# Optimization experiments

Measured on AMD Instinct MI355X. Metric: run time of the kernel, lower is better.

The kernel has to match this reference:

```python
import jax, jax.numpy as jnp
import numpy as np

N = 100000
E = 3200000
IN_CH = 128
HID = 64


def gcn_conv(x, row, col, W, b, n_nodes):
    # PyG GCNConv: add self-loops, symmetric deg^-1/2 normalization,
    # out = scatter_add(norm * (x W)[row] -> col) + bias
    h = x @ W  # [N, out]
    sl = jnp.arange(n_nodes)
    r = jnp.concatenate([row, sl])
    c = jnp.concatenate([col, sl])
    deg = jax.ops.segment_sum(jnp.ones_like(c, dtype=h.dtype), c, num_segments=n_nodes)
    dinv = jnp.where(deg > 0, jax.lax.rsqrt(deg), 0.0)
    norm = dinv[r] * dinv[c]  # [E+N]
    msg = h[r] * norm[:, None]
    out = jax.ops.segment_sum(msg, c, num_segments=n_nodes)
    return out + b


def setup_inputs() -> dict:
    key = jax.random.key(0)
    ks = jax.random.split(key, 8)
    x = jax.random.normal(ks[0], (N, IN_CH), dtype=jnp.float32)
    edge_index = jax.random.randint(ks[1], (2, E), 0, N, dtype=jnp.int64)
    s = 1.0 / np.sqrt(HID)
    W1 = jax.random.normal(ks[2], (IN_CH, HID), dtype=jnp.float32) / np.sqrt(IN_CH)
    b1 = jnp.zeros((HID,), jnp.float32)
    W2 = jax.random.normal(ks[3], (HID, HID), dtype=jnp.float32) * s
    b2 = jnp.zeros((HID,), jnp.float32)
    Wd1 = jax.random.normal(ks[4], (HID, HID), dtype=jnp.float32) * s
    bd1 = jax.random.uniform(ks[5], (HID,), jnp.float32, -s, s)
    Wd2 = jax.random.normal(ks[6], (HID, IN_CH), dtype=jnp.float32) * s
    bd2 = jax.random.uniform(ks[7], (IN_CH,), jnp.float32, -s, s)
    return {"x": x, "edge_index": edge_index, "W1": W1, "b1": b1,
            "W2": W2, "b2": b2, "Wd1": Wd1, "bd1": bd1, "Wd2": Wd2, "bd2": bd2}


def reference(x, edge_index, W1, b1, W2, b2, Wd1, bd1, Wd2, bd2):
    row, col = edge_index[0], edge_index[1]
    h = jax.nn.relu(gcn_conv(x, row, col, W1, b1, N))
    node_representation = jax.nn.relu(gcn_conv(h, row, col, W2, b2, N))
    rec = jax.nn.relu(node_representation @ Wd1 + bd1)
    reconstructed_x = rec @ Wd2 + bd2
    edge_scores = jnp.sum(node_representation[row] * node_representation[col], axis=1)
    return (reconstructed_x, edge_scores, node_representation)
```

## Files before the change

### kernel.cpp

```cpp
#include <hip/hip_runtime.h>

__global__ void k_zero_i(int* __restrict__ p, int n) {
    int i = blockIdx.x * blockDim.x + threadIdx.x;
    if (i < n) p[i] = 0;
}
__global__ void k_zero_f(float* __restrict__ p, long n) {
    long i = blockIdx.x * (long)blockDim.x + threadIdx.x;
    if (i < n) p[i] = 0.0f;
}


#define CH 16384

__global__ void k_hist(const int* __restrict__ col, int* __restrict__ hist,
                       int e, int B, int nchunks) {
    extern __shared__ int lh[];
    for (int i = threadIdx.x; i < B; i += 256) lh[i] = 0;
    __syncthreads();
    const int base = blockIdx.x * CH;
    const int end = min(e, base + CH);
    for (int i = base + threadIdx.x; i < end; i += 256)
        atomicAdd(&lh[col[i] >> 9], 1);
    __syncthreads();
    for (int b = threadIdx.x; b < B; b += 256)
        hist[(long)b * nchunks + blockIdx.x] = lh[b];
}

__global__ void k_scan_tbl(int* __restrict__ hist, long T) {
    __shared__ int ws[1024];
    const int tid = threadIdx.x;
    const long per = (T + 1023) >> 10;
    const long s = tid * per;
    const long e2 = min(T, s + per);
    int sum = 0;
    for (long i = s; i < e2; ++i) sum += hist[i];
    ws[tid] = sum;
    __syncthreads();
    for (int off = 1; off < 1024; off <<= 1) {
        int add = (tid >= off) ? ws[tid - off] : 0;
        __syncthreads();
        ws[tid] += add;
        __syncthreads();
    }
    int run = ws[tid] - sum;
    for (long i = s; i < e2; ++i) { int t = hist[i]; hist[i] = run; run += t; }
}

__global__ void k_part2(const int* __restrict__ row, const int* __restrict__ col,
                        const int* __restrict__ hist, int2* __restrict__ eb,
                        int e, int B, int nchunks) {
    extern __shared__ int cur[];
    const int bId = blockIdx.x;
    for (int b = threadIdx.x; b < B; b += 256)
        cur[b] = hist[(long)b * nchunks + bId];
    __syncthreads();
    const int base = bId * CH;
    const int end = min(e, base + CH);
    for (int i = base + threadIdx.x; i < end; i += 256) {
        int c = col[i];
        int p = atomicAdd(&cur[c >> 9], 1);
        eb[p] = make_int2(row[i], ((c & 511) << 22) | i);
    }
}

__global__ void k_bucket_csr(const int2* __restrict__ eb, const int* __restrict__ hist,
                             int nchunks, int* __restrict__ srow, int* __restrict__ seid,
                             int* __restrict__ startp, float* __restrict__ dinv,
                             int n, int e, int B) {
    __shared__ int scnt[512];
    __shared__ int sex[512];
    const int b = blockIdx.x;
    const int tid = threadIdx.x;
    for (int i = tid; i < 512; i += 256) scnt[i] = 0;
    __syncthreads();
    const int s = hist[(long)b * nchunks];
    const int s1 = (b + 1 < B) ? hist[(long)(b + 1) * nchunks] : e;
    for (int i = s + tid; i < s1; i += 256)
        atomicAdd(&scnt[(eb[i].y >> 22) & 511], 1);
    __syncthreads();
    if (tid < 64) {
        int vals[8];
        int tot = 0;
        #pragma unroll
        for (int k = 0; k < 8; ++k) { vals[k] = scnt[tid * 8 + k]; tot += vals[k]; }
        int acc = tot;
        #pragma unroll
        for (int off = 1; off < 64; off <<= 1) {
            int t = __shfl_up(acc, off);
            if (tid >= off) acc += t;
        }
        int excl = acc - tot;
        #pragma unroll
        for (int k = 0; k < 8; ++k) {
            sex[tid * 8 + k] = excl;
            int node = b * 512 + tid * 8 + k;
            if (node < n) {
                startp[node] = s + excl;
                dinv[node] = rsqrtf((float)vals[k] + 1.0f);
            }
            excl += vals[k];
        }
    }
    if (b == 0 && tid == 0) startp[n] = e;
    __syncthreads();
    for (int i = tid; i < 512; i += 256) scnt[i] = sex[i];
    __syncthreads();
    for (int i = s + tid; i < s1; i += 256) {
        int2 r = eb[i];
        int cl = (r.y >> 22) & 511;
        int p = atomicAdd(&scnt[cl], 1);
        srow[s + p] = r.x;
        seid[s + p] = r.y & 0x3FFFFF;
    }
}

__global__ void k_deg_count(const int* __restrict__ col, int* __restrict__ cnt, int e) {
    int i = blockIdx.x * blockDim.x + threadIdx.x;
    if (i < e) atomicAdd(&cnt[col[i]], 1);
}
__global__ void k_dinv(const int* __restrict__ cnt, float* __restrict__ dinv, int n) {
    int i = blockIdx.x * blockDim.x + threadIdx.x;
    if (i < n) dinv[i] = rsqrtf((float)cnt[i] + 1.0f);
}

template<int K, int OUT, bool BIAS, bool RELU, bool SCALE>
__launch_bounds__(256)
__global__ void k_gemm(const float* __restrict__ in, const float* __restrict__ W,
                       const float* __restrict__ b, const float* __restrict__ scale,
                       float* __restrict__ out, int n) {
    constexpr int NPB = 1024 / OUT;
    constexpr int GS  = 256 / OUT;
    __shared__ float sW[K * OUT];
    __shared__ float sX[NPB][K + 4];

    const int tid  = threadIdx.x;
    const int base = blockIdx.x * NPB;

    for (int i = tid; i < K * OUT; i += 256) sW[i] = W[i];
    for (int i = tid; i < NPB * K; i += 256) {
        int m = i / K, k = i - m * K;
        int node = base + m;
        sX[m][k] = (node < n) ? in[(long)node * K + k] : 0.0f;
    }
    __syncthreads();

    const int ch = tid % OUT;
    const int g  = tid / OUT;

    float acc[4] = {0.f, 0.f, 0.f, 0.f};
    #pragma unroll 4
    for (int k = 0; k < K; k += 4) {
        float w0 = sW[(k + 0) * OUT + ch];
        float w1 = sW[(k + 1) * OUT + ch];
        float w2 = sW[(k + 2) * OUT + ch];
        float w3 = sW[(k + 3) * OUT + ch];
        #pragma unroll
        for (int j = 0; j < 4; ++j) {
            float4 x4 = *reinterpret_cast<const float4*>(&sX[g + j * GS][k]);
            acc[j] += x4.x * w0 + x4.y * w1 + x4.z * w2 + x4.w * w3;
        }
    }

    #pragma unroll
    for (int j = 0; j < 4; ++j) {
        int node = base + g + j * GS;
        if (node < n) {
            float v = acc[j];
            if (BIAS) v += b[ch];
            if (RELU) v = fmaxf(v, 0.0f);
            if (SCALE) v *= scale[node];
            out[(long)node * OUT + ch] = v;
        }
    }
}

__launch_bounds__(256)
__global__ void k_gather_conv(const int* __restrict__ start, const int* __restrict__ srow,
                              const float* __restrict__ hs, const float* __restrict__ dinv,
                              const float* __restrict__ b, float* __restrict__ out, int n) {
    int node = blockIdx.x * 4 + (threadIdx.x >> 6);
    if (node >= n) return;
    int lane = threadIdx.x & 63;
    int sub = lane & 15;
    int eg  = lane >> 4;
    const int s = start[node], e2 = start[node + 1];
    float ax = 0.f, ay = 0.f, az = 0.f, aw = 0.f;
    int j = s + eg;
    for (; j + 28 < e2; j += 32) {
        int r0 = srow[j];      int r1 = srow[j + 4];
        int r2 = srow[j + 8];  int r3 = srow[j + 12];
        int r4 = srow[j + 16]; int r5 = srow[j + 20];
        int r6 = srow[j + 24]; int r7 = srow[j + 28];
        float4 a0 = *reinterpret_cast<const float4*>(&hs[(long)r0 * 64 + sub * 4]);
        float4 a1 = *reinterpret_cast<const float4*>(&hs[(long)r1 * 64 + sub * 4]);
        float4 a2 = *reinterpret_cast<const float4*>(&hs[(long)r2 * 64 + sub * 4]);
        float4 a3 = *reinterpret_cast<const float4*>(&hs[(long)r3 * 64 + sub * 4]);
        float4 a4 = *reinterpret_cast<const float4*>(&hs[(long)r4 * 64 + sub * 4]);
        float4 a5 = *reinterpret_cast<const float4*>(&hs[(long)r5 * 64 + sub * 4]);
        float4 a6 = *reinterpret_cast<const float4*>(&hs[(long)r6 * 64 + sub * 4]);
        float4 a7 = *reinterpret_cast<const float4*>(&hs[(long)r7 * 64 + sub * 4]);
        ax += a0.x; ay += a0.y; az += a0.z; aw += a0.w;
        ax += a1.x; ay += a1.y; az += a1.z; aw += a1.w;
        ax += a2.x; ay += a2.y; az += a2.z; aw += a2.w;
        ax += a3.x; ay += a3.y; az += a3.z; aw += a3.w;
        ax += a4.x; ay += a4.y; az += a4.z; aw += a4.w;
        ax += a5.x; ay += a5.y; az += a5.z; aw += a5.w;
        ax += a6.x; ay += a6.y; az += a6.z; aw += a6.w;
        ax += a7.x; ay += a7.y; az += a7.z; aw += a7.w;
    }
    for (; j < e2; j += 4) {
        int r = srow[j];
        float4 a = *reinterpret_cast<const float4*>(&hs[(long)r * 64 + sub * 4]);
        ax += a.x; ay += a.y; az += a.z; aw += a.w;
    }
    ax += __shfl_xor(ax, 16); ay += __shfl_xor(ay, 16);
    az += __shfl_xor(az, 16); aw += __shfl_xor(aw, 16);
    ax += __shfl_xor(ax, 32); ay += __shfl_xor(ay, 32);
    az += __shfl_xor(az, 32); aw += __shfl_xor(aw, 32);
    if (eg == 0) {
        float4 self = *reinterpret_cast<const float4*>(&hs[(long)node * 64 + sub * 4]);
        float4 b4   = *reinterpret_cast<const float4*>(&b[sub * 4]);
        float d = dinv[node];
        float4 o;
        o.x = fmaxf((ax + self.x) * d + b4.x, 0.0f);
        o.y = fmaxf((ay + self.y) * d + b4.y, 0.0f);
        o.z = fmaxf((az + self.z) * d + b4.z, 0.0f);
        o.w = fmaxf((aw + self.w) * d + b4.w, 0.0f);
        *reinterpret_cast<float4*>(&out[(long)node * 64 + sub * 4]) = o;
    }
}

__launch_bounds__(256)
__global__ void k_edge_scores_csr(const int* __restrict__ start, const int* __restrict__ srow,
                                  const int* __restrict__ eid, const float* __restrict__ nr,
                                  float* __restrict__ out, int n) {
    int node = blockIdx.x * 4 + (threadIdx.x >> 6);
    if (node >= n) return;
    int lane = threadIdx.x & 63;
    int sub = lane & 15;
    int eg  = lane >> 4;
    float4 c4 = *reinterpret_cast<const float4*>(&nr[(long)node * 64 + sub * 4]);
    int s = start[node], e2 = start[node + 1];
    int j = s + eg;
    for (; j + 28 < e2; j += 32) {
        int r0 = srow[j];      int r1 = srow[j + 4];
        int r2 = srow[j + 8];  int r3 = srow[j + 12];
        int r4 = srow[j + 16]; int r5 = srow[j + 20];
        int r6 = srow[j + 24]; int r7 = srow[j + 28];
        float4 a0 = *reinterpret_cast<const float4*>(&nr[(long)r0 * 64 + sub * 4]);
        float4 a1 = *reinterpret_cast<const float4*>(&nr[(long)r1 * 64 + sub * 4]);
        float4 a2 = *reinterpret_cast<const float4*>(&nr[(long)r2 * 64 + sub * 4]);
        float4 a3 = *reinterpret_cast<const float4*>(&nr[(long)r3 * 64 + sub * 4]);
        float4 a4 = *reinterpret_cast<const float4*>(&nr[(long)r4 * 64 + sub * 4]);
        float4 a5 = *reinterpret_cast<const float4*>(&nr[(long)r5 * 64 + sub * 4]);
        float4 a6 = *reinterpret_cast<const float4*>(&nr[(long)r6 * 64 + sub * 4]);
        float4 a7 = *reinterpret_cast<const float4*>(&nr[(long)r7 * 64 + sub * 4]);
        float v0 = a0.x * c4.x + a0.y * c4.y + a0.z * c4.z + a0.w * c4.w;
        float v1 = a1.x * c4.x + a1.y * c4.y + a1.z * c4.z + a1.w * c4.w;
        float v2 = a2.x * c4.x + a2.y * c4.y + a2.z * c4.z + a2.w * c4.w;
        float v3 = a3.x * c4.x + a3.y * c4.y + a3.z * c4.z + a3.w * c4.w;
        float v4 = a4.x * c4.x + a4.y * c4.y + a4.z * c4.z + a4.w * c4.w;
        float v5 = a5.x * c4.x + a5.y * c4.y + a5.z * c4.z + a5.w * c4.w;
        float v6 = a6.x * c4.x + a6.y * c4.y + a6.z * c4.z + a6.w * c4.w;
        float v7 = a7.x * c4.x + a7.y * c4.y + a7.z * c4.z + a7.w * c4.w;
        v0 += __shfl_xor(v0, 1); v1 += __shfl_xor(v1, 1);
        v2 += __shfl_xor(v2, 1); v3 += __shfl_xor(v3, 1);
        v4 += __shfl_xor(v4, 1); v5 += __shfl_xor(v5, 1);
        v6 += __shfl_xor(v6, 1); v7 += __shfl_xor(v7, 1);
        v0 += __shfl_xor(v0, 2); v1 += __shfl_xor(v1, 2);
        v2 += __shfl_xor(v2, 2); v3 += __shfl_xor(v3, 2);
        v4 += __shfl_xor(v4, 2); v5 += __shfl_xor(v5, 2);
        v6 += __shfl_xor(v6, 2); v7 += __shfl_xor(v7, 2);
        v0 += __shfl_xor(v0, 4); v1 += __shfl_xor(v1, 4);
        v2 += __shfl_xor(v2, 4); v3 += __shfl_xor(v3, 4);
        v4 += __shfl_xor(v4, 4); v5 += __shfl_xor(v5, 4);
        v6 += __shfl_xor(v6, 4); v7 += __shfl_xor(v7, 4);
        v0 += __shfl_xor(v0, 8); v1 += __shfl_xor(v1, 8);
        v2 += __shfl_xor(v2, 8); v3 += __shfl_xor(v3, 8);
        v4 += __shfl_xor(v4, 8); v5 += __shfl_xor(v5, 8);
        v6 += __shfl_xor(v6, 8); v7 += __shfl_xor(v7, 8);
        if (sub == 0) {
            out[eid[j]]      = v0; out[eid[j + 4]]  = v1;
            out[eid[j + 8]]  = v2; out[eid[j + 12]] = v3;
            out[eid[j + 16]] = v4; out[eid[j + 20]] = v5;
            out[eid[j + 24]] = v6; out[eid[j + 28]] = v7;
        }
    }
    for (; j + 12 < e2; j += 16) {
        int r0 = srow[j];
        int r1 = srow[j + 4];
        int r2 = srow[j + 8];
        int r3 = srow[j + 12];
        float4 a0 = *reinterpret_cast<const float4*>(&nr[(long)r0 * 64 + sub * 4]);
        float4 a1 = *reinterpret_cast<const float4*>(&nr[(long)r1 * 64 + sub * 4]);
        float4 a2 = *reinterpret_cast<const float4*>(&nr[(long)r2 * 64 + sub * 4]);
        float4 a3 = *reinterpret_cast<const float4*>(&nr[(long)r3 * 64 + sub * 4]);
        float v0 = a0.x * c4.x + a0.y * c4.y + a0.z * c4.z + a0.w * c4.w;
        float v1 = a1.x * c4.x + a1.y * c4.y + a1.z * c4.z + a1.w * c4.w;
        float v2 = a2.x * c4.x + a2.y * c4.y + a2.z * c4.z + a2.w * c4.w;
        float v3 = a3.x * c4.x + a3.y * c4.y + a3.z * c4.z + a3.w * c4.w;
        v0 += __shfl_xor(v0, 1); v1 += __shfl_xor(v1, 1);
        v2 += __shfl_xor(v2, 1); v3 += __shfl_xor(v3, 1);
        v0 += __shfl_xor(v0, 2); v1 += __shfl_xor(v1, 2);
        v2 += __shfl_xor(v2, 2); v3 += __shfl_xor(v3, 2);
        v0 += __shfl_xor(v0, 4); v1 += __shfl_xor(v1, 4);
        v2 += __shfl_xor(v2, 4); v3 += __shfl_xor(v3, 4);
        v0 += __shfl_xor(v0, 8); v1 += __shfl_xor(v1, 8);
        v2 += __shfl_xor(v2, 8); v3 += __shfl_xor(v3, 8);
        if (sub == 0) {
            out[eid[j]]      = v0;
            out[eid[j + 4]]  = v1;
            out[eid[j + 8]]  = v2;
            out[eid[j + 12]] = v3;
        }
    }
    for (; j < e2; j += 4) {
        int r = srow[j];
        float4 a = *reinterpret_cast<const float4*>(&nr[(long)r * 64 + sub * 4]);
        float v = a.x * c4.x + a.y * c4.y + a.z * c4.z + a.w * c4.w;
        v += __shfl_xor(v, 1);
        v += __shfl_xor(v, 2);
        v += __shfl_xor(v, 4);
        v += __shfl_xor(v, 8);
        if (sub == 0) out[eid[j]] = v;
    }
}

__global__ void k_scatter_simple(const int* __restrict__ row, const int* __restrict__ col,
                                 const float* __restrict__ hs, float* __restrict__ acc, int e) {
    int t = blockIdx.x * blockDim.x + threadIdx.x;
    int lane = t & 63;
    int eidx = t >> 6;
    if (eidx >= e) return;
    int r = row[eidx], c = col[eidx];
    atomicAdd(&acc[(long)c * 64 + lane], hs[(long)r * 64 + lane]);
}
__global__ void k_epilogue2(float* __restrict__ acc, const float* __restrict__ hs,
                            const float* __restrict__ dinv, const float* __restrict__ b, int n) {
    int i = blockIdx.x * blockDim.x + threadIdx.x;
    if (i >= n * 64) return;
    int node = i >> 6, ch = i & 63;
    acc[i] = fmaxf(dinv[node] * (acc[i] + hs[i]) + b[ch], 0.0f);
}
__global__ void k_edge_scores_orig(const int* __restrict__ row, const int* __restrict__ col,
                                   const float* __restrict__ nr, float* __restrict__ out, int e) {
    int t = blockIdx.x * blockDim.x + threadIdx.x;
    int sub = t & 15;
    int eidx = t >> 4;
    if (eidx >= e) return;
    int r = row[eidx], c = col[eidx];
    float4 a  = *reinterpret_cast<const float4*>(&nr[(long)r * 64 + sub * 4]);
    float4 bb = *reinterpret_cast<const float4*>(&nr[(long)c * 64 + sub * 4]);
    float s = a.x * bb.x + a.y * bb.y + a.z * bb.z + a.w * bb.w;
    s += __shfl_xor(s, 1);
    s += __shfl_xor(s, 2);
    s += __shfl_xor(s, 4);
    s += __shfl_xor(s, 8);
    if (sub == 0) out[eidx] = s;
}

extern "C" void kernel_launch(void* const* d_in, const int* in_sizes, int n_in,
                              void* d_out, int out_size, void* d_ws, size_t ws_size,
                              hipStream_t stream) {
    const float* x   = (const float*)d_in[0];
    const int*   ei  = (const int*)d_in[1];
    const float* W1  = (const float*)d_in[2];
    const float* b1  = (const float*)d_in[3];
    const float* W2  = (const float*)d_in[4];
    const float* b2  = (const float*)d_in[5];
    const float* Wd1 = (const float*)d_in[6];
    const float* bd1 = (const float*)d_in[7];
    const float* Wd2 = (const float*)d_in[8];
    const float* bd2 = (const float*)d_in[9];

    const int N = in_sizes[0] / 128;
    const int E = in_sizes[1] / 2;
    const int* row = ei;
    const int* col = ei + E;
    const int n64 = N * 64;
    const int B = (N + 511) >> 9;
    const int nchunks = (E + CH - 1) / CH;

    float* recon_out  = (float*)d_out;
    float* escore_out = recon_out + (long)N * 128;
    float* nr_out     = escore_out + E;

    float* dinv = (float*)d_ws;
    float* buf1 = dinv + N;
    float* buf2 = buf1 + (long)N * 64;
    int* startp = (int*)(buf2 + (long)N * 64);
    int* srow   = startp + N + 1;
    int* seid   = srow + E;
    int* hist   = seid + E;
    int2* ebuck = (int2*)buf1;

    size_t need_full = sizeof(float) * ((size_t)N + 2uL * n64)
                     + sizeof(int) * ((size_t)N + 1 + 2uL * E + (size_t)B * nchunks);
    bool csr_ok = (ws_size >= need_full) && (E < (1 << 22)) && ((long)E * 2 <= (long)n64)
                  && (B <= 2048);

    if (csr_ok) {
        k_hist<<<nchunks, 256, B * sizeof(int), stream>>>(col, hist, E, B, nchunks);
        k_scan_tbl<<<1, 1024, 0, stream>>>(hist, (long)B * nchunks);
        k_part2<<<nchunks, 256, B * sizeof(int), stream>>>(row, col, hist, ebuck, E, B, nchunks);
        k_bucket_csr<<<B, 256, 0, stream>>>(ebuck, hist, nchunks, srow, seid, startp, dinv, N, E, B);

        k_gemm<128, 64, false, false, true><<<(N + 15) / 16, 256, 0, stream>>>(x, W1, nullptr, dinv, buf1, N);
        k_gather_conv<<<(N + 3) / 4, 256, 0, stream>>>(startp, srow, buf1, dinv, b1, buf2, N);
        k_gemm<64, 64, false, false, true><<<(N + 15) / 16, 256, 0, stream>>>(buf2, W2, nullptr, dinv, buf1, N);
        k_gather_conv<<<(N + 3) / 4, 256, 0, stream>>>(startp, srow, buf1, dinv, b2, nr_out, N);
        k_gemm<64, 64, true, true, false><<<(N + 15) / 16, 256, 0, stream>>>(nr_out, Wd1, bd1, nullptr, buf2, N);
        k_gemm<64, 128, true, false, false><<<(N + 7) / 8, 256, 0, stream>>>(buf2, Wd2, bd2, nullptr, recon_out, N);
        k_edge_scores_csr<<<(N + 3) / 4, 256, 0, stream>>>(startp, srow, seid, nr_out, escore_out, N);
    } else {
        int* cnt = startp;
        k_zero_i<<<(N + 255) / 256, 256, 0, stream>>>(cnt, N);
        k_deg_count<<<(E + 255) / 256, 256, 0, stream>>>(col, cnt, E);
        k_dinv<<<(N + 255) / 256, 256, 0, stream>>>(cnt, dinv, N);
        k_zero_f<<<(n64 + 255) / 256, 256, 0, stream>>>(buf2, n64);
        k_zero_f<<<(n64 + 255) / 256, 256, 0, stream>>>(nr_out, n64);

        k_gemm<128, 64, false, false, true><<<(N + 15) / 16, 256, 0, stream>>>(x, W1, nullptr, dinv, buf1, N);
        k_scatter_simple<<<((long)E * 64 + 255) / 256, 256, 0, stream>>>(row, col, buf1, buf2, E);
        k_epilogue2<<<(n64 + 255) / 256, 256, 0, stream>>>(buf2, buf1, dinv, b1, N);
        k_gemm<64, 64, false, false, true><<<(N + 15) / 16, 256, 0, stream>>>(buf2, W2, nullptr, dinv, buf1, N);
        k_scatter_simple<<<((long)E * 64 + 255) / 256, 256, 0, stream>>>(row, col, buf1, nr_out, E);
        k_epilogue2<<<(n64 + 255) / 256, 256, 0, stream>>>(nr_out, buf1, dinv, b2, N);
        k_gemm<64, 64, true, true, false><<<(N + 15) / 16, 256, 0, stream>>>(nr_out, Wd1, bd1, nullptr, buf2, N);
        k_gemm<64, 128, true, false, false><<<(N + 7) / 8, 256, 0, stream>>>(buf2, Wd2, bd2, nullptr, recon_out, N);
        k_edge_scores_orig<<<((long)E * 16 + 255) / 256, 256, 0, stream>>>(row, col, nr_out, escore_out, E);
    }
}
```

Measured before the change: 915.3 us.

## Fuse W2 GEMM into first gather-conv and fuse both decoder GEMMs

The second-layer weight multiply (W2, scaled by dinv) moves into the epilogue of the first aggregation kernel. Each block stages W2 in shared memory and multiplies its 4 aggregated rows there, which removes one intermediate round trip to global memory and one launch. The two decoder GEMMs are merged into one kernel that keeps the ReLU hidden layer in shared memory. The cost is that every 4-node gather block now reloads 16KB of W2 and every 8-node decoder block reloads 48KB of weights, which adds shared-memory and L2 traffic and may lower occupancy.

```diff
diff --git a/kernel.cpp b/kernel.cpp
--- a/kernel.cpp
+++ b/kernel.cpp
@@ -171,6 +171,85 @@
             if (SCALE) v *= scale[node];
             out[(long)node * OUT + ch] = v;
         }
+    }
+}
+
+__launch_bounds__(256)
+__global__ void k_gather_conv_w2(const int* __restrict__ start, const int* __restrict__ srow,
+                                 const float* __restrict__ hs, const float* __restrict__ dinv,
+                                 const float* __restrict__ b, const float* __restrict__ W2,
+                                 float* __restrict__ hs2, int n) {
+    __shared__ float sW[64 * 64];
+    __shared__ float srb[4][64];
+    const int tid = threadIdx.x;
+    for (int i = tid; i < 64 * 64; i += 256) sW[i] = W2[i];
+
+    const int wid = tid >> 6;
+    const int node = blockIdx.x * 4 + wid;
+    const bool valid = node < n;
+    const int lane = tid & 63;
+    const int sub = lane & 15;
+    const int eg  = lane >> 4;
+
+    int s = 0, e2 = 0;
+    if (valid) { s = start[node]; e2 = start[node + 1]; }
+    float ax = 0.f, ay = 0.f, az = 0.f, aw = 0.f;
+    int j = s + eg;
+    for (; j + 28 < e2; j += 32) {
+        int r0 = srow[j];      int r1 = srow[j + 4];
+        int r2 = srow[j + 8];  int r3 = srow[j + 12];
+        int r4 = srow[j + 16]; int r5 = srow[j + 20];
+        int r6 = srow[j + 24]; int r7 = srow[j + 28];
+        float4 a0 = *reinterpret_cast<const float4*>(&hs[(long)r0 * 64 + sub * 4]);
+        float4 a1 = *reinterpret_cast<const float4*>(&hs[(long)r1 * 64 + sub * 4]);
+        float4 a2 = *reinterpret_cast<const float4*>(&hs[(long)r2 * 64 + sub * 4]);
+        float4 a3 = *reinterpret_cast<const float4*>(&hs[(long)r3 * 64 + sub * 4]);
+        float4 a4 = *reinterpret_cast<const float4*>(&hs[(long)r4 * 64 + sub * 4]);
+        float4 a5 = *reinterpret_cast<const float4*>(&hs[(long)r5 * 64 + sub * 4]);
+        float4 a6 = *reinterpret_cast<const float4*>(&hs[(long)r6 * 64 + sub * 4]);
+        float4 a7 = *reinterpret_cast<const float4*>(&hs[(long)r7 * 64 + sub * 4]);
+        ax += a0.x; ay += a0.y; az += a0.z; aw += a0.w;
+        ax += a1.x; ay += a1.y; az += a1.z; aw += a1.w;
+        ax += a2.x; ay += a2.y; az += a2.z; aw += a2.w;
+        ax += a3.x; ay += a3.y; az += a3.z; aw += a3.w;
+        ax += a4.x; ay += a4.y; az += a4.z; aw += a4.w;
+        ax += a5.x; ay += a5.y; az += a5.z; aw += a5.w;
+        ax += a6.x; ay += a6.y; az += a6.z; aw += a6.w;
+        ax += a7.x; ay += a7.y; az += a7.z; aw += a7.w;
+    }
+    for (; j < e2; j += 4) {
+        int r = srow[j];
+        float4 a = *reinterpret_cast<const float4*>(&hs[(long)r * 64 + sub * 4]);
+        ax += a.x; ay += a.y; az += a.z; aw += a.w;
+    }
+    ax += __shfl_xor(ax, 16); ay += __shfl_xor(ay, 16);
+    az += __shfl_xor(az, 16); aw += __shfl_xor(aw, 16);
+    ax += __shfl_xor(ax, 32); ay += __shfl_xor(ay, 32);
+    az += __shfl_xor(az, 32); aw += __shfl_xor(aw, 32);
+
+    float d = valid ? dinv[node] : 0.f;
+    if (valid && eg == 0) {
+        float4 self = *reinterpret_cast<const float4*>(&hs[(long)node * 64 + sub * 4]);
+        float4 b4   = *reinterpret_cast<const float4*>(&b[sub * 4]);
+        float4 o;
+        o.x = fmaxf((ax + self.x) * d + b4.x, 0.0f);
+        o.y = fmaxf((ay + self.y) * d + b4.y, 0.0f);
+        o.z = fmaxf((az + self.z) * d + b4.z, 0.0f);
+        o.w = fmaxf((aw + self.w) * d + b4.w, 0.0f);
+        *reinterpret_cast<float4*>(&srb[wid][sub * 4]) = o;
+    }
+    __syncthreads();
+    if (valid) {
+        float acc = 0.f;
+        #pragma unroll 4
+        for (int k = 0; k < 64; k += 4) {
+            float4 r4 = *reinterpret_cast<const float4*>(&srb[wid][k]);
+            acc += r4.x * sW[(k + 0) * 64 + lane];
+            acc += r4.y * sW[(k + 1) * 64 + lane];
+            acc += r4.z * sW[(k + 2) * 64 + lane];
+            acc += r4.w * sW[(k + 3) * 64 + lane];
+        }
+        hs2[(long)node * 64 + lane] = acc * d;
     }
 }
 
@@ -227,6 +306,72 @@
         o.z = fmaxf((az + self.z) * d + b4.z, 0.0f);
         o.w = fmaxf((aw + self.w) * d + b4.w, 0.0f);
         *reinterpret_cast<float4*>(&out[(long)node * 64 + sub * 4]) = o;
+    }
+}
+
+__launch_bounds__(256)
+__global__ void k_decoder(const float* __restrict__ nr, const float* __restrict__ Wd1,
+                          const float* __restrict__ bd1, const float* __restrict__ Wd2,
+                          const float* __restrict__ bd2, float* __restrict__ recon, int n) {
+    __shared__ float sW1[64 * 64];
+    __shared__ float sW2d[64 * 128];
+    __shared__ float sX[8][68];
+    __shared__ float sR[8][68];
+    const int tid = threadIdx.x;
+    const int base = blockIdx.x * 8;
+    for (int i = tid; i < 64 * 64; i += 256) sW1[i] = Wd1[i];
+    for (int i = tid; i < 64 * 128; i += 256) sW2d[i] = Wd2[i];
+    for (int i = tid; i < 8 * 64; i += 256) {
+        int m = i >> 6, k = i & 63;
+        int node = base + m;
+        sX[m][k] = (node < n) ? nr[(long)node * 64 + k] : 0.0f;
+    }
+    __syncthreads();
+    {
+        const int ch = tid & 63;
+        const int g  = tid >> 6;
+        float acc0 = 0.f, acc1 = 0.f;
+        #pragma unroll 4
+        for (int k = 0; k < 64; k += 4) {
+            float w0 = sW1[(k + 0) * 64 + ch];
+            float w1 = sW1[(k + 1) * 64 + ch];
+            float w2 = sW1[(k + 2) * 64 + ch];
+            float w3 = sW1[(k + 3) * 64 + ch];
+            float4 x0 = *reinterpret_cast<const float4*>(&sX[g][k]);
+            float4 x1 = *reinterpret_cast<const float4*>(&sX[g + 4][k]);
+            acc0 += x0.x * w0 + x0.y * w1 + x0.z * w2 + x0.w * w3;
+            acc1 += x1.x * w0 + x1.y * w1 + x1.z * w2 + x1.w * w3;
+        }
+        float bb = bd1[ch];
+        sR[g][ch]     = fmaxf(acc0 + bb, 0.f);
+        sR[g + 4][ch] = fmaxf(acc1 + bb, 0.f);
+    }
+    __syncthreads();
+    {
+        const int ch = tid & 127;
+        const int g2 = tid >> 7;
+        float a0 = 0.f, a1 = 0.f, a2 = 0.f, a3 = 0.f;
+        #pragma unroll 4
+        for (int k = 0; k < 64; k += 4) {
+            float w0 = sW2d[(k + 0) * 128 + ch];
+            float w1 = sW2d[(k + 1) * 128 + ch];
+            float w2 = sW2d[(k + 2) * 128 + ch];
+            float w3 = sW2d[(k + 3) * 128 + ch];
+            float4 r0 = *reinterpret_cast<const float4*>(&sR[g2][k]);
+            float4 r1 = *reinterpret_cast<const float4*>(&sR[g2 + 2][k]);
+            float4 r2 = *reinterpret_cast<const float4*>(&sR[g2 + 4][k]);
+            float4 r3 = *reinterpret_cast<const float4*>(&sR[g2 + 6][k]);
+            a0 += r0.x * w0 + r0.y * w1 + r0.z * w2 + r0.w * w3;
+            a1 += r1.x * w0 + r1.y * w1 + r1.z * w2 + r1.w * w3;
+            a2 += r2.x * w0 + r2.y * w1 + r2.z * w2 + r2.w * w3;
+            a3 += r3.x * w0 + r3.y * w1 + r3.z * w2 + r3.w * w3;
+        }
+        float bb = bd2[ch];
+        int n0 = base + g2;
+        if (n0 < n)     recon[(long)n0 * 128 + ch]       = a0 + bb;
+        if (n0 + 2 < n) recon[(long)(n0 + 2) * 128 + ch] = a1 + bb;
+        if (n0 + 4 < n) recon[(long)(n0 + 4) * 128 + ch] = a2 + bb;
+        if (n0 + 6 < n) recon[(long)(n0 + 6) * 128 + ch] = a3 + bb;
     }
 }
 
@@ -406,11 +551,9 @@
         k_bucket_csr<<<B, 256, 0, stream>>>(ebuck, hist, nchunks, srow, seid, startp, dinv, N, E, B);
 
         k_gemm<128, 64, false, false, true><<<(N + 15) / 16, 256, 0, stream>>>(x, W1, nullptr, dinv, buf1, N);
-        k_gather_conv<<<(N + 3) / 4, 256, 0, stream>>>(startp, srow, buf1, dinv, b1, buf2, N);
-        k_gemm<64, 64, false, false, true><<<(N + 15) / 16, 256, 0, stream>>>(buf2, W2, nullptr, dinv, buf1, N);
-        k_gather_conv<<<(N + 3) / 4, 256, 0, stream>>>(startp, srow, buf1, dinv, b2, nr_out, N);
-        k_gemm<64, 64, true, true, false><<<(N + 15) / 16, 256, 0, stream>>>(nr_out, Wd1, bd1, nullptr, buf2, N);
-        k_gemm<64, 128, true, false, false><<<(N + 7) / 8, 256, 0, stream>>>(buf2, Wd2, bd2, nullptr, recon_out, N);
+        k_gather_conv_w2<<<(N + 3) / 4, 256, 0, stream>>>(startp, srow, buf1, dinv, b1, W2, buf2, N);
+        k_gather_conv<<<(N + 3) / 4, 256, 0, stream>>>(startp, srow, buf2, dinv, b2, nr_out, N);
+        k_decoder<<<(N + 7) / 8, 256, 0, stream>>>(nr_out, Wd1, bd1, Wd2, bd2, recon_out, N);
         k_edge_scores_csr<<<(N + 3) / 4, 256, 0, stream>>>(startp, srow, seid, nr_out, escore_out, N);
     } else {
         int* cnt = startp;
```

After: 933.2 us. Within noise of the previous version (+2.0%).
